# Kernel tuning notes

Hardware: AMD Instinct MI355X
Metric: run time of the kernel (lower is better)

Reference implementation:

```python
import jax, jax.numpy as jnp
import numpy as np

BS, C_IN, H, W = 16, 128, 64, 64
C_OUT, K, STRIDE, PAD, DIL = 256, 3, 1, 1, 1
ALPHA = 0.5  # scaling_factor
QMAX = 127.0  # int8 symmetric fake-quant


def _fake_quant(t):
    # symmetric per-tensor int8 fake quantization with straight-through estimator
    s = jax.lax.stop_gradient(jnp.max(jnp.abs(t))) / QMAX
    s = jnp.where(s == 0, 1.0, s)
    q = jnp.clip(jnp.round(t / s), -QMAX, QMAX) * s
    return t + jax.lax.stop_gradient(q - t)  # STE


def setup_inputs() -> dict:
    key = jax.random.key(0)
    k1, k2, k3 = jax.random.split(key, 3)
    x = jax.random.normal(k1, (BS, C_IN, H, W), dtype=jnp.float32)
    weight = jax.random.normal(k2, (C_OUT, C_IN, K, K), dtype=jnp.float32) * 0.05
    bias = jax.random.normal(k3, (C_OUT,), dtype=jnp.float32) * 0.01
    return {"x": x, "weight": weight, "bias": bias}


def reference(x, weight, bias):
    bs, _, h_in, w_in = x.shape
    ickhkw = C_IN * K * K
    h_out = (h_in + 2 * PAD - DIL * (K - 1) - 1) // STRIDE + 1
    w_out = (w_in + 2 * PAD - DIL * (K - 1) - 1) // STRIDE + 1

    # im2col (matches torch F.unfold feature ordering: channel-major, then kh, kw)
    patches = jax.lax.conv_general_dilated_patches(
        x, filter_shape=(K, K), window_strides=(STRIDE, STRIDE),
        padding=((PAD, PAD), (PAD, PAD)), rhs_dilation=(DIL, DIL),
    )  # [bs, ickhkw, h_out, w_out]
    cols = patches.reshape(bs, ickhkw, h_out * w_out)
    cols = cols.transpose(0, 2, 1).reshape(-1, ickhkw)  # [bs*L, ickhkw]

    w2 = weight.reshape(C_OUT, ickhkw)

    # SmoothQuant per-column scales (detached)
    w_scale = jax.lax.stop_gradient(jnp.max(jnp.abs(w2), axis=0))    # [ickhkw]
    act_scale = jax.lax.stop_gradient(jnp.max(jnp.abs(cols), axis=0))  # [ickhkw]
    scale = act_scale ** ALPHA / w_scale ** (1.0 - ALPHA)
    scale = jnp.where(scale == 0, 1.0, scale)

    w_s = _fake_quant(w2 * scale)
    x_s = _fake_quant(cols / scale)

    out = x_s @ w_s.T  # [bs*L, C_OUT]
    out = out.reshape(bs, h_out * w_out, C_OUT).transpose(0, 2, 1)
    out = out.reshape(bs, C_OUT, h_out, w_out)
    return out + bias.reshape(1, C_OUT, 1, 1)
```

## Files before the change

### kernel.cpp

```cpp
#include <hip/hip_runtime.h>
#include <cstdint>

#define C_IN   128
#define C_OUT  256
#define KK     1152
#define NPIX   4096
#define BS     16
#define M_ROWS 65536
#define QMAXF  127.0f

typedef int v4i __attribute__((ext_vector_type(4)));

#define OFF_QW    75497472
#define OFF_SCALE 75792384
#define OFF_QMUL  75796992
#define OFF_APART 75801600
#define OFF_SCAL  75843072

__global__ void k_prep(const float* __restrict__ x, const float* __restrict__ wgt,
                       float* __restrict__ act_part, float* __restrict__ w_part) {
    const int tid = threadIdx.x;
    if (blockIdx.x >= 1024) {
        int t = blockIdx.x - 1024;
        int j = (t % 5) * 256 + tid;
        int s = t / 5;
        if (j >= KK) return;
        const float* p = wgt + (size_t)s * 16 * KK + j;
        float m = 0.f;
#pragma unroll
        for (int i = 0; i < 16; i++) m = fmaxf(m, fabsf(p[(size_t)i * KK]));
        w_part[s * KK + j] = m;
        return;
    }
    const int c = blockIdx.x >> 3, s = blockIdx.x & 7;
    float m[9];
#pragma unroll
    for (int i = 0; i < 9; i++) m[i] = 0.f;
    for (int p = tid; p < 2 * NPIX; p += 256) {
        int b = s * 2 + (p >> 12);
        int hw = p & 4095;
        int h = hw >> 6, w = hw & 63;
        float v = fabsf(x[b * (C_IN * NPIX) + c * NPIX + hw]);
        bool rr[3] = { h <= 62, true, h >= 1 };
        bool cc[3] = { w <= 62, true, w >= 1 };
#pragma unroll
        for (int i = 0; i < 3; i++)
#pragma unroll
            for (int jq = 0; jq < 3; jq++)
                m[i * 3 + jq] = fmaxf(m[i * 3 + jq], (rr[i] && cc[jq]) ? v : 0.f);
    }
    __shared__ float sm[9][4];
    int lane = tid & 63, wid = tid >> 6;
#pragma unroll
    for (int i = 0; i < 9; i++) {
        float v = m[i];
        for (int off = 32; off > 0; off >>= 1) v = fmaxf(v, __shfl_down(v, off));
        if (lane == 0) sm[i][wid] = v;
    }
    __syncthreads();
    if (tid < 9) {
        float v = fmaxf(fmaxf(sm[tid][0], sm[tid][1]), fmaxf(sm[tid][2], sm[tid][3]));
        act_part[s * KK + c * 9 + tid] = v;
    }
}

__global__ void k_scales(const float* __restrict__ act_part, const float* __restrict__ w_part,
                         float* __restrict__ scale, float* __restrict__ qmul,
                         float* __restrict__ scalars) {
    const int tid = threadIdx.x;
    float sc_local[2] = {1.f, 1.f};
    float mx = 0.f, mw = 0.f;
#pragma unroll
    for (int t = 0; t < 2; t++) {
        int j = tid + t * 1024;
        if (j < KK) {
            float a = 0.f;
#pragma unroll
            for (int s = 0; s < 8; s++) a = fmaxf(a, act_part[s * KK + j]);
            float wv = 0.f;
#pragma unroll
            for (int s = 0; s < 16; s++) wv = fmaxf(wv, w_part[s * KK + j]);
            float sc = sqrtf(a) / sqrtf(wv);
            if (sc == 0.f) sc = 1.0f;
            scale[j] = sc;
            sc_local[t] = sc;
            mx = fmaxf(mx, a / sc);
            mw = fmaxf(mw, wv * sc);
        }
    }
    __shared__ float smx[16], smw[16];
    __shared__ float s_x_sh;
    int lane = tid & 63, wid = tid >> 6;
    for (int off = 32; off > 0; off >>= 1) {
        mx = fmaxf(mx, __shfl_down(mx, off));
        mw = fmaxf(mw, __shfl_down(mw, off));
    }
    if (lane == 0) { smx[wid] = mx; smw[wid] = mw; }
    __syncthreads();
    if (tid == 0) {
        float a = 0.f, b = 0.f;
        for (int i = 0; i < 16; i++) { a = fmaxf(a, smx[i]); b = fmaxf(b, smw[i]); }
        float s_x = a / QMAXF; if (s_x == 0.f) s_x = 1.f;
        float s_w = b / QMAXF; if (s_w == 0.f) s_w = 1.f;
        scalars[0] = s_x; scalars[1] = s_w; scalars[2] = s_x * s_w;
        s_x_sh = s_x;
    }
    __syncthreads();
    float s_x = s_x_sh;
#pragma unroll
    for (int t = 0; t < 2; t++) {
        int j = tid + t * 1024;
        if (j < KK) qmul[j] = 1.0f / (sc_local[t] * s_x);
    }
}

__global__ void k_quant_w(const float* __restrict__ wgt, const float* __restrict__ scale,
                          const float* __restrict__ scalars, signed char* __restrict__ qWp) {
    int idx = blockIdx.x * 256 + threadIdx.x;
    int m  = (unsigned)idx / KK;
    int kp = idx - m * KK;
    int tap = kp >> 7, c = kp & 127;
    int j = c * 9 + tap;
    float s_w = scalars[1];
    float t = wgt[m * KK + j] * scale[j];
    float q = rintf(t / s_w);
    q = fminf(fmaxf(q, -QMAXF), QMAXF);
    qWp[idx] = (signed char)(int)q;
}

__global__ __launch_bounds__(512, 4) void k_gemm(const signed char* __restrict__ qWp,
                                                 const float* __restrict__ x,
                                                 const float* __restrict__ qmul,
                                                 const float* __restrict__ scalars,
                                                 const float* __restrict__ bias,
                                                 float* __restrict__ out) {
    __shared__ __align__(16) signed char Bs[2][64 * 128];
    __shared__ float qm[KK];
    const int tid = threadIdx.x;
    const int lane = tid & 63, wv = tid >> 6;
    const int b  = blockIdx.x >> 6;
    const int oh = blockIdx.x & 63;
    const float* xb = x + (size_t)b * (C_IN * NPIX);
    const int c0 = wv * 16;

    for (int i = tid; i < KK; i += 512) {
        int tap = i >> 7, c = i & 127;
        qm[i] = qmul[c * 9 + tap];
    }

    const signed char* aBase = qWp + (size_t)(wv * 32 + (lane & 15)) * KK + (lane >> 4) * 16;

    v4i acc[2][4];
#pragma unroll
    for (int i = 0; i < 2; i++)
#pragma unroll
        for (int jq = 0; jq < 4; jq++) acc[i][jq] = (v4i){0, 0, 0, 0};

    float xr[16], xrn[16];
    {
        const bool ok = oh >= 1;
        const float* s = xb + (oh - 1) * 64 + lane;
#pragma unroll
        for (int d = 0; d < 16; d++) xr[d] = ok ? s[(size_t)(c0 + d) * NPIX] : 0.f;
    }
    v4i af[2][2], afn[2][2];
#pragma unroll
    for (int h = 0; h < 2; h++)
#pragma unroll
        for (int mt = 0; mt < 2; mt++)
            af[h][mt] = *(const v4i*)(aBase + (size_t)mt * 16 * KK + 0 * 128 + h * 64);

    __syncthreads();

#pragma unroll
    for (int tap = 0; tap < 9; tap++) {
        const int g  = (tap * 11) >> 5;
        const int jj = tap - g * 3;
        const int s  = jj - 1;
        const bool rowok = ((unsigned)(oh - 1 + g)) < 64u;
        signed char* bsp = (signed char*)Bs[tap & 1];

        {
            int n = lane - s;
            bool valid = (unsigned)n < 64u;
            int wrow = valid ? n : (s == -1 ? 0 : 63);
            bool live = rowok && valid;
            const float* qmt = qm + tap * 128 + c0;
            int pk[4];
#pragma unroll
            for (int d4 = 0; d4 < 4; d4++) {
                int w = 0;
#pragma unroll
                for (int e = 0; e < 4; e++) {
                    float v = live ? xr[d4 * 4 + e] : 0.f;
                    float q = rintf(v * qmt[d4 * 4 + e]);
                    q = fminf(fmaxf(q, -QMAXF), QMAXF);
                    w |= ((int)q & 255) << (8 * e);
                }
                pk[d4] = w;
            }
            *(v4i*)(bsp + wrow * 128 + ((wv ^ (wrow & 7)) * 16)) = (v4i){pk[0], pk[1], pk[2], pk[3]};
        }

        if (jj == 0 && g < 2) {
            const bool ok = (unsigned)(oh + g) < 64u;
            const float* sp = xb + (oh + g) * 64 + lane;
#pragma unroll
            for (int d = 0; d < 16; d++) xrn[d] = ok ? sp[(size_t)(c0 + d) * NPIX] : 0.f;
        }

        __syncthreads();

        if (tap < 8) {
#pragma unroll
            for (int h = 0; h < 2; h++)
#pragma unroll
                for (int mt = 0; mt < 2; mt++)
                    afn[h][mt] = *(const v4i*)(aBase + (size_t)mt * 16 * KK + (tap + 1) * 128 + h * 64);
        }

#pragma unroll
        for (int h = 0; h < 2; h++) {
            const int q4 = h * 4 + (lane >> 4);
            v4i bf[4];
#pragma unroll
            for (int nt = 0; nt < 4; nt++) {
                int rb = nt * 16 + (lane & 15);
                bf[nt] = *(const v4i*)(bsp + rb * 128 + ((q4 ^ (rb & 7)) * 16));
            }
#pragma unroll
            for (int mt = 0; mt < 2; mt++)
#pragma unroll
                for (int nt = 0; nt < 4; nt++)
                    acc[mt][nt] = __builtin_amdgcn_mfma_i32_16x16x64_i8(af[h][mt], bf[nt], acc[mt][nt], 0, 0, 0);
        }

        if (tap < 8) {
#pragma unroll
            for (int h = 0; h < 2; h++)
#pragma unroll
                for (int mt = 0; mt < 2; mt++) af[h][mt] = afn[h][mt];
        }
        if (jj == 2 && g < 2) {
#pragma unroll
            for (int d = 0; d < 16; d++) xr[d] = xrn[d];
        }
    }

    const float ssp = scalars[2];
    const int quad = lane >> 4, col = lane & 15;
    float bv[2][4];
#pragma unroll
    for (int mt = 0; mt < 2; mt++)
#pragma unroll
        for (int rg = 0; rg < 4; rg++)
            bv[mt][rg] = bias[wv * 32 + mt * 16 + quad * 4 + rg];

    float* obase = out + ((size_t)b * C_OUT) * NPIX + oh * 64;
#pragma unroll
    for (int mt = 0; mt < 2; mt++) {
#pragma unroll
        for (int nt = 0; nt < 4; nt++) {
            int n = nt * 16 + col;
#pragma unroll
            for (int rg = 0; rg < 4; rg++) {
                int m = wv * 32 + mt * 16 + quad * 4 + rg;
                obase[(size_t)m * NPIX + n] = (float)acc[mt][nt][rg] * ssp + bv[mt][rg];
            }
        }
    }
}

extern "C" void kernel_launch(void* const* d_in, const int* in_sizes, int n_in,
                              void* d_out, int out_size, void* d_ws, size_t ws_size,
                              hipStream_t stream) {
    const float* x    = (const float*)d_in[0];
    const float* wgt  = (const float*)d_in[1];
    const float* bias = (const float*)d_in[2];
    float* out = (float*)d_out;

    char* ws = (char*)d_ws;
    signed char* qWp = (signed char*)(ws + OFF_QW);
    float* w_part    = (float*)(ws + OFF_QW);
    float* scale     = (float*)(ws + OFF_SCALE);
    float* qmul      = (float*)(ws + OFF_QMUL);
    float* act_part  = (float*)(ws + OFF_APART);
    float* scalars   = (float*)(ws + OFF_SCAL);

    k_prep<<<1104, 256, 0, stream>>>(x, wgt, act_part, w_part);
    k_scales<<<1, 1024, 0, stream>>>(act_part, w_part, scale, qmul, scalars);
    k_quant_w<<<(C_OUT * KK) / 256, 256, 0, stream>>>(wgt, scale, scalars, qWp);
    k_gemm<<<BS * 64, 512, 0, stream>>>(qWp, x, qmul, scalars, bias, out);
}
```

Measured before the change: 159.0 us.

## Software-pipeline tap loop: quantize next tap's B tile while MFMAs consume current

Restructures the 9-tap loop so the quantize-and-store of tap t+1 into the alternate shared buffer overlaps with the MFMA work on tap t. This cuts one barrier-separated produce/consume phase per iteration. Input row loads are rescheduled: the center row is loaded in the prologue and the next row at t==2, with xr/xrn roles swapped by row group. It adds register pressure and more complex buffer indexing.

```diff
diff --git a/kernel.cpp b/kernel.cpp
--- a/kernel.cpp
+++ b/kernel.cpp
@@ -127,6 +127,32 @@
     q = fminf(fmaxf(q, -QMAXF), QMAXF);
     qWp[idx] = (signed char)(int)q;
 }
+
+#define PRODUCE(TP, XV, BSP)                                                    \
+    do {                                                                        \
+        const int g_ = (TP) / 3, jj_ = (TP) - g_ * 3, sh_ = jj_ - 1;            \
+        const bool rowok_ = ((unsigned)(oh - 1 + g_)) < 64u;                    \
+        int n_ = lane - sh_;                                                    \
+        bool valid_ = (unsigned)n_ < 64u;                                       \
+        int wrow_ = valid_ ? n_ : (sh_ == -1 ? 0 : 63);                         \
+        bool live_ = rowok_ && valid_;                                          \
+        const float* qmt_ = qm + (TP) * 128 + c0;                               \
+        int pk_[4];                                                             \
+        _Pragma("unroll")                                                       \
+        for (int d4 = 0; d4 < 4; d4++) {                                        \
+            int w_ = 0;                                                         \
+            _Pragma("unroll")                                                   \
+            for (int e = 0; e < 4; e++) {                                       \
+                float v_ = live_ ? XV[d4 * 4 + e] : 0.f;                        \
+                float q_ = rintf(v_ * qmt_[d4 * 4 + e]);                        \
+                q_ = fminf(fmaxf(q_, -QMAXF), QMAXF);                           \
+                w_ |= ((int)q_ & 255) << (8 * e);                               \
+            }                                                                   \
+            pk_[d4] = w_;                                                       \
+        }                                                                       \
+        *(v4i*)((BSP) + wrow_ * 128 + ((wv ^ (wrow_ & 7)) * 16)) =              \
+            (v4i){pk_[0], pk_[1], pk_[2], pk_[3]};                              \
+    } while (0)
 
 __global__ __launch_bounds__(512, 4) void k_gemm(const signed char* __restrict__ qWp,
                                                  const float* __restrict__ x,
@@ -172,78 +198,76 @@
 
     __syncthreads();
 
-#pragma unroll
-    for (int tap = 0; tap < 9; tap++) {
-        const int g  = (tap * 11) >> 5;
-        const int jj = tap - g * 3;
-        const int s  = jj - 1;
-        const bool rowok = ((unsigned)(oh - 1 + g)) < 64u;
-        signed char* bsp = (signed char*)Bs[tap & 1];
-
-        {
-            int n = lane - s;
-            bool valid = (unsigned)n < 64u;
-            int wrow = valid ? n : (s == -1 ? 0 : 63);
-            bool live = rowok && valid;
-            const float* qmt = qm + tap * 128 + c0;
-            int pk[4];
-#pragma unroll
-            for (int d4 = 0; d4 < 4; d4++) {
-                int w = 0;
-#pragma unroll
-                for (int e = 0; e < 4; e++) {
-                    float v = live ? xr[d4 * 4 + e] : 0.f;
-                    float q = rintf(v * qmt[d4 * 4 + e]);
-                    q = fminf(fmaxf(q, -QMAXF), QMAXF);
-                    w |= ((int)q & 255) << (8 * e);
-                }
-                pk[d4] = w;
-            }
-            *(v4i*)(bsp + wrow * 128 + ((wv ^ (wrow & 7)) * 16)) = (v4i){pk[0], pk[1], pk[2], pk[3]};
-        }
-
-        if (jj == 0 && g < 2) {
-            const bool ok = (unsigned)(oh + g) < 64u;
-            const float* sp = xb + (oh + g) * 64 + lane;
-#pragma unroll
-            for (int d = 0; d < 16; d++) xrn[d] = ok ? sp[(size_t)(c0 + d) * NPIX] : 0.f;
-        }
-
-        __syncthreads();
-
-        if (tap < 8) {
+    PRODUCE(0, xr, (signed char*)Bs[0]);
+
+    {
+        const float* sp = xb + oh * 64 + lane;
+#pragma unroll
+        for (int d = 0; d < 16; d++) xrn[d] = sp[(size_t)(c0 + d) * NPIX];
+    }
+
+    __syncthreads();
+
+#pragma unroll
+    for (int t = 0; t < 9; t++) {
+        const signed char* bsR = (const signed char*)Bs[t & 1];
+        signed char* bsW = (signed char*)Bs[(t + 1) & 1];
+
+        v4i bf0[4];
+#pragma unroll
+        for (int nt = 0; nt < 4; nt++) {
+            int rb = nt * 16 + (lane & 15);
+            int q4 = (lane >> 4);
+            bf0[nt] = *(const v4i*)(bsR + rb * 128 + ((q4 ^ (rb & 7)) * 16));
+        }
+
+        if (t < 8) {
 #pragma unroll
             for (int h = 0; h < 2; h++)
 #pragma unroll
                 for (int mt = 0; mt < 2; mt++)
-                    afn[h][mt] = *(const v4i*)(aBase + (size_t)mt * 16 * KK + (tap + 1) * 128 + h * 64);
-        }
-
-#pragma unroll
-        for (int h = 0; h < 2; h++) {
-            const int q4 = h * 4 + (lane >> 4);
-            v4i bf[4];
-#pragma unroll
-            for (int nt = 0; nt < 4; nt++) {
-                int rb = nt * 16 + (lane & 15);
-                bf[nt] = *(const v4i*)(bsp + rb * 128 + ((q4 ^ (rb & 7)) * 16));
-            }
-#pragma unroll
-            for (int mt = 0; mt < 2; mt++)
-#pragma unroll
-                for (int nt = 0; nt < 4; nt++)
-                    acc[mt][nt] = __builtin_amdgcn_mfma_i32_16x16x64_i8(af[h][mt], bf[nt], acc[mt][nt], 0, 0, 0);
-        }
-
-        if (tap < 8) {
+                    afn[h][mt] = *(const v4i*)(aBase + (size_t)mt * 16 * KK + (t + 1) * 128 + h * 64);
+        }
+
+        if (t == 2) {
+            const bool ok = (oh + 1) < 64;
+            const float* sp = xb + (oh + 1) * 64 + lane;
+#pragma unroll
+            for (int d = 0; d < 16; d++) xr[d] = ok ? sp[(size_t)(c0 + d) * NPIX] : 0.f;
+        }
+
+        if (t < 8) {
+            const int tap = t + 1;
+            const int g = tap / 3;
+            if (g == 1) PRODUCE(tap, xrn, bsW);
+            else        PRODUCE(tap, xr,  bsW);
+        }
+
+#pragma unroll
+        for (int mt = 0; mt < 2; mt++)
+#pragma unroll
+            for (int nt = 0; nt < 4; nt++)
+                acc[mt][nt] = __builtin_amdgcn_mfma_i32_16x16x64_i8(af[0][mt], bf0[nt], acc[mt][nt], 0, 0, 0);
+
+        v4i bf1[4];
+#pragma unroll
+        for (int nt = 0; nt < 4; nt++) {
+            int rb = nt * 16 + (lane & 15);
+            int q4 = 4 + (lane >> 4);
+            bf1[nt] = *(const v4i*)(bsR + rb * 128 + ((q4 ^ (rb & 7)) * 16));
+        }
+#pragma unroll
+        for (int mt = 0; mt < 2; mt++)
+#pragma unroll
+            for (int nt = 0; nt < 4; nt++)
+                acc[mt][nt] = __builtin_amdgcn_mfma_i32_16x16x64_i8(af[1][mt], bf1[nt], acc[mt][nt], 0, 0, 0);
+
+        if (t < 8) {
 #pragma unroll
             for (int h = 0; h < 2; h++)
 #pragma unroll
                 for (int mt = 0; mt < 2; mt++) af[h][mt] = afn[h][mt];
-        }
-        if (jj == 2 && g < 2) {
-#pragma unroll
-            for (int d = 0; d < 16; d++) xr[d] = xrn[d];
+            __syncthreads();
         }
     }
 
```

Result: slower. 171.9 us (+8.1%).

## Split GEMM blocks over output-channel halves, vectorize act-max scan, simplify quant packing

Applied to the files above, without the earlier changes.

The GEMM kernel now launches twice as many 256-thread blocks. Each block computes half of the output channels, with a swizzled block index so that neighbouring blocks are spread across XCDs. Each wave now quantizes 32 input channels, packs bytes with perm instructions and drops the clamp, and loads A fragments in the loop without prefetching, adding a second barrier per tap. The prep kernel reads x with float4 loads. This trades twice the on-the-fly activation quantization work for more blocks and lower register pressure, and removes the row-boundary check on top/bottom taps, which may need verification.

```diff
diff --git a/kernel.cpp b/kernel.cpp
--- a/kernel.cpp
+++ b/kernel.cpp
@@ -36,18 +36,26 @@
     float m[9];
 #pragma unroll
     for (int i = 0; i < 9; i++) m[i] = 0.f;
-    for (int p = tid; p < 2 * NPIX; p += 256) {
-        int b = s * 2 + (p >> 12);
-        int hw = p & 4095;
-        int h = hw >> 6, w = hw & 63;
-        float v = fabsf(x[b * (C_IN * NPIX) + c * NPIX + hw]);
+    const float4* xp4 = (const float4*)(x + (size_t)(s * 2) * (C_IN * NPIX) + (size_t)c * NPIX);
+    const int img4 = C_IN * NPIX / 4;
+    for (int v = tid; v < 2048; v += 256) {
+        int half = v >> 10;
+        int hw4  = v & 1023;
+        int h  = hw4 >> 4;
+        int w4 = (hw4 & 15) * 4;
+        float4 f = xp4[half * img4 + hw4];
         bool rr[3] = { h <= 62, true, h >= 1 };
-        bool cc[3] = { w <= 62, true, w >= 1 };
-#pragma unroll
-        for (int i = 0; i < 3; i++)
-#pragma unroll
-            for (int jq = 0; jq < 3; jq++)
-                m[i * 3 + jq] = fmaxf(m[i * 3 + jq], (rr[i] && cc[jq]) ? v : 0.f);
+#pragma unroll
+        for (int e = 0; e < 4; e++) {
+            int w = w4 + e;
+            float vv = fabsf(e == 0 ? f.x : e == 1 ? f.y : e == 2 ? f.z : f.w);
+            bool cc[3] = { w <= 62, true, w >= 1 };
+#pragma unroll
+            for (int i = 0; i < 3; i++)
+#pragma unroll
+                for (int jq = 0; jq < 3; jq++)
+                    m[i * 3 + jq] = fmaxf(m[i * 3 + jq], (rr[i] && cc[jq]) ? vv : 0.f);
+        }
     }
     __shared__ float sm[9][4];
     int lane = tid & 63, wid = tid >> 6;
@@ -128,7 +136,34 @@
     qWp[idx] = (signed char)(int)q;
 }
 
-__global__ __launch_bounds__(512, 4) void k_gemm(const signed char* __restrict__ qWp,
+#define PRODUCE(TP, BSP)                                                        \
+    do {                                                                        \
+        const int jj_ = (TP) % 3, sh_ = jj_ - 1;                                \
+        int n_ = lane - sh_;                                                    \
+        bool valid_ = (unsigned)n_ < 64u;                                       \
+        int wrow_ = valid_ ? n_ : (sh_ == -1 ? 0 : 63);                         \
+        _Pragma("unroll")                                                       \
+        for (int ha = 0; ha < 2; ha++) {                                        \
+            const float* qmt_ = qm + (TP) * 128 + c0 + ha * 16;                 \
+            const float* xv_ = xr + ha * 16;                                    \
+            int pk_[4];                                                         \
+            _Pragma("unroll")                                                   \
+            for (int d4 = 0; d4 < 4; d4++) {                                    \
+                int q0_ = (int)rintf(xv_[d4 * 4 + 0] * qmt_[d4 * 4 + 0]);       \
+                int q1_ = (int)rintf(xv_[d4 * 4 + 1] * qmt_[d4 * 4 + 1]);       \
+                int q2_ = (int)rintf(xv_[d4 * 4 + 2] * qmt_[d4 * 4 + 2]);       \
+                int q3_ = (int)rintf(xv_[d4 * 4 + 3] * qmt_[d4 * 4 + 3]);       \
+                unsigned t0_ = __builtin_amdgcn_perm((unsigned)q1_, (unsigned)q0_, 0x0c0c0400u); \
+                unsigned t1_ = __builtin_amdgcn_perm((unsigned)q3_, (unsigned)q2_, 0x0c0c0400u); \
+                int w_ = (int)__builtin_amdgcn_perm(t1_, t0_, 0x05040100u);     \
+                pk_[d4] = valid_ ? w_ : 0;                                      \
+            }                                                                   \
+            *(v4i*)((BSP) + wrow_ * 128 + (((wv * 2 + ha) ^ (wrow_ & 7)) * 16)) = \
+                (v4i){pk_[0], pk_[1], pk_[2], pk_[3]};                          \
+        }                                                                       \
+    } while (0)
+
+__global__ __launch_bounds__(256, 4) void k_gemm(const signed char* __restrict__ qWp,
                                                  const float* __restrict__ x,
                                                  const float* __restrict__ qmul,
                                                  const float* __restrict__ scalars,
@@ -138,17 +173,20 @@
     __shared__ float qm[KK];
     const int tid = threadIdx.x;
     const int lane = tid & 63, wv = tid >> 6;
-    const int b  = blockIdx.x >> 6;
-    const int oh = blockIdx.x & 63;
+    const int raw = blockIdx.x;
+    const int swz = (raw & 7) * 256 + (raw >> 3);
+    const int b  = swz >> 7;
+    const int oh = (swz >> 1) & 63;
+    const int hm = swz & 1;
     const float* xb = x + (size_t)b * (C_IN * NPIX);
-    const int c0 = wv * 16;
-
-    for (int i = tid; i < KK; i += 512) {
+    const int c0 = wv * 32;
+
+    for (int i = tid; i < KK; i += 256) {
         int tap = i >> 7, c = i & 127;
         qm[i] = qmul[c * 9 + tap];
     }
 
-    const signed char* aBase = qWp + (size_t)(wv * 32 + (lane & 15)) * KK + (lane >> 4) * 16;
+    const signed char* aBase = qWp + (size_t)(hm * 128 + wv * 32 + (lane & 15)) * KK + (lane >> 4) * 16;
 
     v4i acc[2][4];
 #pragma unroll
@@ -156,68 +194,42 @@
 #pragma unroll
         for (int jq = 0; jq < 4; jq++) acc[i][jq] = (v4i){0, 0, 0, 0};
 
-    float xr[16], xrn[16];
+    float xr[32];
     {
         const bool ok = oh >= 1;
         const float* s = xb + (oh - 1) * 64 + lane;
 #pragma unroll
-        for (int d = 0; d < 16; d++) xr[d] = ok ? s[(size_t)(c0 + d) * NPIX] : 0.f;
-    }
-    v4i af[2][2], afn[2][2];
-#pragma unroll
-    for (int h = 0; h < 2; h++)
-#pragma unroll
-        for (int mt = 0; mt < 2; mt++)
-            af[h][mt] = *(const v4i*)(aBase + (size_t)mt * 16 * KK + 0 * 128 + h * 64);
-
-    __syncthreads();
-
-#pragma unroll
-    for (int tap = 0; tap < 9; tap++) {
-        const int g  = (tap * 11) >> 5;
-        const int jj = tap - g * 3;
-        const int s  = jj - 1;
-        const bool rowok = ((unsigned)(oh - 1 + g)) < 64u;
-        signed char* bsp = (signed char*)Bs[tap & 1];
-
-        {
-            int n = lane - s;
-            bool valid = (unsigned)n < 64u;
-            int wrow = valid ? n : (s == -1 ? 0 : 63);
-            bool live = rowok && valid;
-            const float* qmt = qm + tap * 128 + c0;
-            int pk[4];
-#pragma unroll
-            for (int d4 = 0; d4 < 4; d4++) {
-                int w = 0;
-#pragma unroll
-                for (int e = 0; e < 4; e++) {
-                    float v = live ? xr[d4 * 4 + e] : 0.f;
-                    float q = rintf(v * qmt[d4 * 4 + e]);
-                    q = fminf(fmaxf(q, -QMAXF), QMAXF);
-                    w |= ((int)q & 255) << (8 * e);
-                }
-                pk[d4] = w;
-            }
-            *(v4i*)(bsp + wrow * 128 + ((wv ^ (wrow & 7)) * 16)) = (v4i){pk[0], pk[1], pk[2], pk[3]};
-        }
-
-        if (jj == 0 && g < 2) {
-            const bool ok = (unsigned)(oh + g) < 64u;
-            const float* sp = xb + (oh + g) * 64 + lane;
-#pragma unroll
-            for (int d = 0; d < 16; d++) xrn[d] = ok ? sp[(size_t)(c0 + d) * NPIX] : 0.f;
+        for (int d = 0; d < 32; d++) xr[d] = ok ? s[(size_t)(c0 + d) * NPIX] : 0.f;
+    }
+    v4i af[2][2];
+
+    __syncthreads();
+
+#pragma unroll
+    for (int t = 0; t < 9; t++) {
+        signed char* bsp = (signed char*)Bs[t & 1];
+
+#pragma unroll
+        for (int h = 0; h < 2; h++)
+#pragma unroll
+            for (int mt = 0; mt < 2; mt++)
+                af[h][mt] = *(const v4i*)(aBase + (size_t)mt * 16 * KK + t * 128 + h * 64);
+
+        PRODUCE(t, bsp);
+
+        if (t == 2) {
+            const float* sp = xb + oh * 64 + lane;
+#pragma unroll
+            for (int d = 0; d < 32; d++) xr[d] = sp[(size_t)(c0 + d) * NPIX];
+        }
+        if (t == 5) {
+            const bool ok = (oh + 1) < 64;
+            const float* sp = xb + (oh + 1) * 64 + lane;
+#pragma unroll
+            for (int d = 0; d < 32; d++) xr[d] = ok ? sp[(size_t)(c0 + d) * NPIX] : 0.f;
         }
 
         __syncthreads();
-
-        if (tap < 8) {
-#pragma unroll
-            for (int h = 0; h < 2; h++)
-#pragma unroll
-                for (int mt = 0; mt < 2; mt++)
-                    afn[h][mt] = *(const v4i*)(aBase + (size_t)mt * 16 * KK + (tap + 1) * 128 + h * 64);
-        }
 
 #pragma unroll
         for (int h = 0; h < 2; h++) {
@@ -235,16 +247,7 @@
                     acc[mt][nt] = __builtin_amdgcn_mfma_i32_16x16x64_i8(af[h][mt], bf[nt], acc[mt][nt], 0, 0, 0);
         }
 
-        if (tap < 8) {
-#pragma unroll
-            for (int h = 0; h < 2; h++)
-#pragma unroll
-                for (int mt = 0; mt < 2; mt++) af[h][mt] = afn[h][mt];
-        }
-        if (jj == 2 && g < 2) {
-#pragma unroll
-            for (int d = 0; d < 16; d++) xr[d] = xrn[d];
-        }
+        if (t < 8) __syncthreads();
     }
 
     const float ssp = scalars[2];
@@ -254,7 +257,7 @@
     for (int mt = 0; mt < 2; mt++)
 #pragma unroll
         for (int rg = 0; rg < 4; rg++)
-            bv[mt][rg] = bias[wv * 32 + mt * 16 + quad * 4 + rg];
+            bv[mt][rg] = bias[hm * 128 + wv * 32 + mt * 16 + quad * 4 + rg];
 
     float* obase = out + ((size_t)b * C_OUT) * NPIX + oh * 64;
 #pragma unroll
@@ -264,7 +267,7 @@
             int n = nt * 16 + col;
 #pragma unroll
             for (int rg = 0; rg < 4; rg++) {
-                int m = wv * 32 + mt * 16 + quad * 4 + rg;
+                int m = hm * 128 + wv * 32 + mt * 16 + quad * 4 + rg;
                 obase[(size_t)m * NPIX + n] = (float)acc[mt][nt][rg] * ssp + bv[mt][rg];
             }
         }
@@ -290,5 +293,5 @@
     k_prep<<<1104, 256, 0, stream>>>(x, wgt, act_part, w_part);
     k_scales<<<1, 1024, 0, stream>>>(act_part, w_part, scale, qmul, scalars);
     k_quant_w<<<(C_OUT * KK) / 256, 256, 0, stream>>>(wgt, scale, scalars, qWp);
-    k_gemm<<<BS * 64, 512, 0, stream>>>(qWp, x, qmul, scalars, bias, out);
-}
+    k_gemm<<<2 * BS * 64, 256, 0, stream>>>(qWp, x, qmul, scalars, bias, out);
+}
```

Measured after the change: 147.9 us. -7.0%, faster.
